# Kernel optimization log

Measured on AMD Instinct MI355X. Metric: run time of the kernel, lower is better.

## Reference

```python
import jax, jax.numpy as jnp
import numpy as np

D_MODEL = 256; HEADS = 8; DHEAD = D_MODEL // HEADS; FF = 2048
B, N = 2, 1024
T, H, W = 16, 128, 128
DS = (2, 8, 8)    # downsample_factor == offset_scale
KS = (4, 10, 10)  # offset kernel size


def layer_norm(x, w, b, eps=1e-5):
    mu = x.mean(-1, keepdims=True)
    var = ((x - mu) ** 2).mean(-1, keepdims=True)
    return (x - mu) * jax.lax.rsqrt(var + eps) * w + b


def mha_self(x, in_w, in_b, out_w, out_b):
    # torch nn.MultiheadAttention (batch_first), self-attention, eval mode
    Bq, Nq, C = x.shape
    qkv = x @ in_w.T + in_b
    q, k, v = jnp.split(qkv, 3, axis=-1)
    sh = lambda t: t.reshape(Bq, Nq, HEADS, DHEAD).transpose(0, 2, 1, 3)
    q, k, v = sh(q), sh(k), sh(v)
    att = jax.nn.softmax(jnp.einsum('bhnd,bhmd->bhnm', q, k) / np.sqrt(DHEAD).astype(np.float32), axis=-1)
    o = jnp.einsum('bhnm,bhmd->bhnd', att, v).transpose(0, 2, 1, 3).reshape(Bq, Nq, C)
    return o @ out_w.T + out_b


def grid_sample_3d(vol, coords):
    # vol: (G,C,T,H,W); coords: (G,L,3) in [-1,1], order (z,y,x)
    # trilinear, zeros padding, align_corners=False (matches F.grid_sample)
    G, C, Tv, Hv, Wv = vol.shape
    z = ((coords[..., 0] + 1.0) * Tv - 1.0) * 0.5
    y = ((coords[..., 1] + 1.0) * Hv - 1.0) * 0.5
    x = ((coords[..., 2] + 1.0) * Wv - 1.0) * 0.5
    z0f, y0f, x0f = jnp.floor(z), jnp.floor(y), jnp.floor(x)
    wz1, wy1, wx1 = z - z0f, y - y0f, x - x0f
    z0, y0, x0 = z0f.astype(jnp.int32), y0f.astype(jnp.int32), x0f.astype(jnp.int32)
    flat = vol.reshape(G, C, Tv * Hv * Wv)

    def gather(zi, yi, xi):
        valid = ((zi >= 0) & (zi < Tv) & (yi >= 0) & (yi < Hv) & (xi >= 0) & (xi < Wv))
        idx = (jnp.clip(zi, 0, Tv - 1) * Hv + jnp.clip(yi, 0, Hv - 1)) * Wv + jnp.clip(xi, 0, Wv - 1)
        vals = jnp.take_along_axis(flat, idx[:, None, :], axis=2)
        return vals * valid[:, None, :].astype(vol.dtype)

    out = jnp.zeros((G, C, coords.shape[1]), vol.dtype)
    for dz in (0, 1):
        for dy in (0, 1):
            for dx in (0, 1):
                w = ((wz1 if dz else 1 - wz1) * (wy1 if dy else 1 - wy1) * (wx1 if dx else 1 - wx1))
                out = out + gather(z0 + dz, y0 + dy, x0 + dx) * w[:, None, :]
    return out


def deform_attn(x, queries, q_w, off_w1, off_b1, off_w2, k_w, v_w, out_w, out_b):
    # DeformableAttention3D: offsets from grouped volume features via strided
    # depthwise conv, tanh*offset_scale, grid_sample of the full-res volume,
    # grouped k/v projections, per-head attention of N queries over L samples.
    Bx, C, Tv, Hv, Wv = x.shape
    g, d = HEADS, C // HEADS
    Nq = queries.shape[1]
    xg = x.reshape(Bx * g, d, Tv, Hv, Wv)
    pads = [((k - s) // 2, (k - s) // 2) for k, s in zip(KS, DS)]
    off = jax.lax.conv_general_dilated(xg, off_w1, window_strides=DS, padding=pads,
                                       dimension_numbers=('NCDHW', 'OIDHW', 'NCDHW'),
                                       feature_group_count=d)
    off = jax.nn.gelu(off + off_b1[None, :, None, None, None])
    off = jnp.einsum('oc,bcthw->bothw', off_w2, off)  # (BG,3,t,h,w)
    scale = jnp.asarray(DS, off.dtype)
    off = jnp.tanh(off) * scale[None, :, None, None, None]
    td, hd, wd = off.shape[2:]
    gz, gy, gx = jnp.meshgrid(jnp.arange(td), jnp.arange(hd), jnp.arange(wd), indexing='ij')
    base = jnp.stack([gz, gy, gx], 0).astype(off.dtype)
    norm = jnp.asarray([max(td - 1, 1), max(hd - 1, 1), max(wd - 1, 1)], off.dtype)
    vgrid = 2.0 * (base[None] + off) / norm[None, :, None, None, None] - 1.0
    coords = vgrid.transpose(0, 2, 3, 4, 1).reshape(Bx * g, -1, 3)  # (BG,L,3)
    kv = grid_sample_3d(xg, coords).reshape(Bx, g, d, -1)            # (B,g,d,L)
    k = jnp.einsum('gof,bgfl->bgol', k_w, kv)
    v = jnp.einsum('gof,bgfl->bgol', v_w, kv)
    q = (queries @ q_w.T).reshape(Bx, Nq, g, d).transpose(0, 2, 1, 3)
    attn = jax.nn.softmax(jnp.einsum('bgnd,bgdl->bgnl', q, k) / np.sqrt(d).astype(np.float32), axis=-1)
    o = jnp.einsum('bgnl,bgdl->bgnd', attn, v).transpose(0, 2, 1, 3).reshape(Bx, Nq, C)
    return o @ out_w.T + out_b, attn


def decoder_layer(query_tokens, global_tokens, p):
    # forward_post, use_pe='use_pe' with pos=None, dropout in eval mode
    t = query_tokens + mha_self(query_tokens, p['sa_in_w'], p['sa_in_b'], p['sa_out_w'], p['sa_out_b'])
    t = layer_norm(t, p['ln1_w'], p['ln1_b'])
    da, attn = deform_attn(global_tokens, t, p['q_w'], p['off_w1'], p['off_b1'], p['off_w2'],
                           p['k_w'], p['v_w'], p['da_out_w'], p['da_out_b'])
    t = layer_norm(t + da, p['ln2_w'], p['ln2_b'])
    ff = jax.nn.relu(t @ p['lin1_w'].T + p['lin1_b']) @ p['lin2_w'].T + p['lin2_b']
    t = layer_norm(t + ff, p['ln3_w'], p['ln3_b'])
    return t, attn


PARAM_NAMES = ['sa_in_w', 'sa_in_b', 'sa_out_w', 'sa_out_b', 'q_w', 'off_w1', 'off_b1', 'off_w2',
               'k_w', 'v_w', 'da_out_w', 'da_out_b', 'lin1_w', 'lin1_b', 'lin2_w', 'lin2_b',
               'ln1_w', 'ln1_b', 'ln2_w', 'ln2_b', 'ln3_w', 'ln3_b']


def setup_inputs() -> dict:
    key = jax.random.key(0)
    ks = jax.random.split(key, 16)
    s = 0.02
    f = jnp.float32
    return {
        'query_tokens': jax.random.normal(ks[0], (B, N, D_MODEL), f),
        'global_tokens': jax.random.normal(ks[1], (B, D_MODEL, T, H, W), f),
        'sa_in_w': jax.random.normal(ks[2], (3 * D_MODEL, D_MODEL), f) * s,
        'sa_in_b': jnp.zeros((3 * D_MODEL,), f),
        'sa_out_w': jax.random.normal(ks[3], (D_MODEL, D_MODEL), f) * s,
        'sa_out_b': jnp.zeros((D_MODEL,), f),
        'q_w': jax.random.normal(ks[4], (D_MODEL, D_MODEL), f) * s,
        'off_w1': jax.random.normal(ks[5], (DHEAD, 1) + KS, f) * s,
        'off_b1': jnp.zeros((DHEAD,), f),
        'off_w2': jax.random.normal(ks[6], (3, DHEAD), f) * s,
        'k_w': jax.random.normal(ks[7], (HEADS, DHEAD, DHEAD), f) * s,
        'v_w': jax.random.normal(ks[8], (HEADS, DHEAD, DHEAD), f) * s,
        'da_out_w': jax.random.normal(ks[9], (D_MODEL, D_MODEL), f) * s,
        'da_out_b': jnp.zeros((D_MODEL,), f),
        'lin1_w': jax.random.normal(ks[10], (FF, D_MODEL), f) * s,
        'lin1_b': jnp.zeros((FF,), f),
        'lin2_w': jax.random.normal(ks[11], (D_MODEL, FF), f) * s,
        'lin2_b': jnp.zeros((D_MODEL,), f),
        'ln1_w': jnp.ones((D_MODEL,), f), 'ln1_b': jnp.zeros((D_MODEL,), f),
        'ln2_w': jnp.ones((D_MODEL,), f), 'ln2_b': jnp.zeros((D_MODEL,), f),
        'ln3_w': jnp.ones((D_MODEL,), f), 'ln3_b': jnp.zeros((D_MODEL,), f),
    }


def reference(query_tokens, global_tokens, sa_in_w, sa_in_b, sa_out_w, sa_out_b, q_w, off_w1,
              off_b1, off_w2, k_w, v_w, da_out_w, da_out_b, lin1_w, lin1_b, lin2_w, lin2_b,
              ln1_w, ln1_b, ln2_w, ln2_b, ln3_w, ln3_b):
    p = dict(zip(PARAM_NAMES, (sa_in_w, sa_in_b, sa_out_w, sa_out_b, q_w, off_w1, off_b1, off_w2,
                               k_w, v_w, da_out_w, da_out_b, lin1_w, lin1_b, lin2_w, lin2_b,
                               ln1_w, ln1_b, ln2_w, ln2_b, ln3_w, ln3_b)))
    return decoder_layer(query_tokens, global_tokens, p)
```

## Files before the change

### kernel.cpp

```cpp
#include <hip/hip_runtime.h>
#include <hip/hip_bf16.h>

#define BQ 2
#define NQ 1024
#define CM 256
#define HEADS 8
#define DH 32
#define FFD 2048
#define TV 16
#define HV 128
#define WV 128
#define TD 8
#define HD 16
#define WD 16
#define LS 2048
#define NG 16
#define MROWS 2048

typedef __attribute__((ext_vector_type(8))) short bf16x8;
typedef __attribute__((ext_vector_type(4))) float f32x4;

__device__ __forceinline__ ushort f2bf(float x) {
  __hip_bfloat16 h = __float2bfloat16(x);
  return *(ushort*)&h;
}

template <bool RELU>
__global__ __launch_bounds__(256) void gemm_nt(const float* __restrict__ A,
                                               const float* __restrict__ Wt,
                                               const float* __restrict__ bias,
                                               const float* __restrict__ res,
                                               float* __restrict__ C,
                                               int M, int N, int K) {
  __shared__ float As[16 * 68];
  __shared__ float Ws[16 * 68];
  const int tm = threadIdx.x & 15;
  const int tn = threadIdx.x >> 4;
  const int m0 = blockIdx.x * 64, n0 = blockIdx.y * 64;
  const int lr = threadIdx.x >> 2;
  const int lk = (threadIdx.x & 3) * 4;
  float acc[4][4] = {};
  for (int k0 = 0; k0 < K; k0 += 16) {
    float4 a4 = *(const float4*)(A + (size_t)(m0 + lr) * K + k0 + lk);
    float4 w4 = *(const float4*)(Wt + (size_t)(n0 + lr) * K + k0 + lk);
    As[(lk + 0) * 68 + lr] = a4.x;
    As[(lk + 1) * 68 + lr] = a4.y;
    As[(lk + 2) * 68 + lr] = a4.z;
    As[(lk + 3) * 68 + lr] = a4.w;
    Ws[(lk + 0) * 68 + lr] = w4.x;
    Ws[(lk + 1) * 68 + lr] = w4.y;
    Ws[(lk + 2) * 68 + lr] = w4.z;
    Ws[(lk + 3) * 68 + lr] = w4.w;
    __syncthreads();
#pragma unroll
    for (int k = 0; k < 16; ++k) {
      float4 av = *(const float4*)&As[k * 68 + tm * 4];
      float4 wv = *(const float4*)&Ws[k * 68 + tn * 4];
      float a[4] = {av.x, av.y, av.z, av.w};
      float w[4] = {wv.x, wv.y, wv.z, wv.w};
#pragma unroll
      for (int i = 0; i < 4; ++i)
#pragma unroll
        for (int j = 0; j < 4; ++j) acc[i][j] += a[i] * w[j];
    }
    __syncthreads();
  }
#pragma unroll
  for (int i = 0; i < 4; ++i) {
    const int row = m0 + tm * 4 + i;
    const int col = n0 + tn * 4;
    float4 bv = bias ? *(const float4*)(bias + col) : make_float4(0.f, 0.f, 0.f, 0.f);
    float4 rv = res ? *(const float4*)(res + (size_t)row * N + col) : make_float4(0.f, 0.f, 0.f, 0.f);
    float4 o;
    o.x = acc[i][0] + bv.x + rv.x;
    o.y = acc[i][1] + bv.y + rv.y;
    o.z = acc[i][2] + bv.z + rv.z;
    o.w = acc[i][3] + bv.w + rv.w;
    if (RELU) {
      o.x = fmaxf(o.x, 0.f); o.y = fmaxf(o.y, 0.f);
      o.z = fmaxf(o.z, 0.f); o.w = fmaxf(o.w, 0.f);
    }
    *(float4*)(C + (size_t)row * N + col) = o;
  }
}

template <bool RELU>
__global__ __launch_bounds__(256) void gemm_nt128(const float* __restrict__ A,
                                                  const float* __restrict__ Wt,
                                                  const float* __restrict__ bias,
                                                  const float* __restrict__ res,
                                                  float* __restrict__ C,
                                                  int M, int N, int K) {
  __shared__ float As[8][132];
  __shared__ float Bs[8][132];
  const int tid = threadIdx.x;
  const int tm = tid & 15, tn = tid >> 4;
  const int m0 = blockIdx.x * 128, n0 = blockIdx.y * 128;
  const int lr = tid >> 1, lk = (tid & 1) * 4;
  float acc[8][8] = {};
  const float* Ap = A + (size_t)(m0 + lr) * K + lk;
  const float* Wp = Wt + (size_t)(n0 + lr) * K + lk;
  for (int k0 = 0; k0 < K; k0 += 8) {
    float4 a4 = *(const float4*)(Ap + k0);
    float4 w4 = *(const float4*)(Wp + k0);
    __syncthreads();
    As[lk + 0][lr] = a4.x; As[lk + 1][lr] = a4.y; As[lk + 2][lr] = a4.z; As[lk + 3][lr] = a4.w;
    Bs[lk + 0][lr] = w4.x; Bs[lk + 1][lr] = w4.y; Bs[lk + 2][lr] = w4.z; Bs[lk + 3][lr] = w4.w;
    __syncthreads();
#pragma unroll
    for (int k = 0; k < 8; ++k) {
      float4 a0 = *(const float4*)&As[k][tm * 8];
      float4 a1 = *(const float4*)&As[k][tm * 8 + 4];
      float4 w0 = *(const float4*)&Bs[k][tn * 8];
      float4 w1 = *(const float4*)&Bs[k][tn * 8 + 4];
      float av[8] = {a0.x, a0.y, a0.z, a0.w, a1.x, a1.y, a1.z, a1.w};
      float wv[8] = {w0.x, w0.y, w0.z, w0.w, w1.x, w1.y, w1.z, w1.w};
#pragma unroll
      for (int i = 0; i < 8; ++i)
#pragma unroll
        for (int j = 0; j < 8; ++j) acc[i][j] += av[i] * wv[j];
    }
  }
#pragma unroll
  for (int i = 0; i < 8; ++i) {
    const int row = m0 + tm * 8 + i;
#pragma unroll
    for (int jj = 0; jj < 2; ++jj) {
      const int col = n0 + tn * 8 + jj * 4;
      float4 o = make_float4(acc[i][jj * 4 + 0], acc[i][jj * 4 + 1],
                             acc[i][jj * 4 + 2], acc[i][jj * 4 + 3]);
      if (bias) {
        float4 bv = *(const float4*)(bias + col);
        o.x += bv.x; o.y += bv.y; o.z += bv.z; o.w += bv.w;
      }
      if (res) {
        float4 rv = *(const float4*)(res + (size_t)row * N + col);
        o.x += rv.x; o.y += rv.y; o.z += rv.z; o.w += rv.w;
      }
      if (RELU) {
        o.x = fmaxf(o.x, 0.f); o.y = fmaxf(o.y, 0.f);
        o.z = fmaxf(o.z, 0.f); o.w = fmaxf(o.w, 0.f);
      }
      *(float4*)(C + (size_t)row * N + col) = o;
    }
  }
}

__global__ __launch_bounds__(256) void castw_kernel(const float* __restrict__ w1,
                                                    const float* __restrict__ w2,
                                                    __hip_bfloat16* __restrict__ w1b,
                                                    __hip_bfloat16* __restrict__ w2b) {
  const int idx = blockIdx.x * 256 + threadIdx.x;
  const float4* src;
  __hip_bfloat16* dst;
  int off;
  if (idx < 131072) { src = (const float4*)w1; dst = w1b; off = idx; }
  else              { src = (const float4*)w2; dst = w2b; off = idx - 131072; }
  float4 v = src[off];
  dst[off * 4 + 0] = __float2bfloat16(v.x);
  dst[off * 4 + 1] = __float2bfloat16(v.y);
  dst[off * 4 + 2] = __float2bfloat16(v.z);
  dst[off * 4 + 3] = __float2bfloat16(v.w);
}

template <bool LIN1>
__global__ __launch_bounds__(256) void gemm_bf16_mfma(const ushort* __restrict__ A,
                                                      const ushort* __restrict__ B,
                                                      const float* __restrict__ bias,
                                                      __hip_bfloat16* __restrict__ Cbf,
                                                      float* __restrict__ Cf,
                                                      int M, int N, int K, int kslen) {
  __shared__ ushort Asm[128][40];
  __shared__ ushort Bsm[128][40];
  const int tid = threadIdx.x;
  const int lane = tid & 63, wave = tid >> 6;
  const int wr = wave >> 1, wc = wave & 1;
  const int m0 = blockIdx.x * 128, n0 = blockIdx.y * 128;
  const int kb = blockIdx.z * kslen;
  f32x4 acc[4][4] = {};

  const int r0 = tid >> 1, c0 = (tid & 1) * 16;
  for (int k0 = kb; k0 < kb + kslen; k0 += 32) {
    uint4 ar0 = *(const uint4*)(A + (size_t)(m0 + r0) * K + k0 + c0);
    uint4 ar1 = *(const uint4*)(A + (size_t)(m0 + r0) * K + k0 + c0 + 8);
    uint4 br0 = *(const uint4*)(B + (size_t)(n0 + r0) * K + k0 + c0);
    uint4 br1 = *(const uint4*)(B + (size_t)(n0 + r0) * K + k0 + c0 + 8);
    __syncthreads();
    *(uint4*)&Asm[r0][c0] = ar0;
    *(uint4*)&Asm[r0][c0 + 8] = ar1;
    *(uint4*)&Bsm[r0][c0] = br0;
    *(uint4*)&Bsm[r0][c0 + 8] = br1;
    __syncthreads();
    bf16x8 af[4], bfr[4];
#pragma unroll
    for (int mi = 0; mi < 4; ++mi)
      af[mi] = *(const bf16x8*)&Asm[wr * 64 + mi * 16 + (lane & 15)][(lane >> 4) * 8];
#pragma unroll
    for (int ni = 0; ni < 4; ++ni)
      bfr[ni] = *(const bf16x8*)&Bsm[wc * 64 + ni * 16 + (lane & 15)][(lane >> 4) * 8];
#pragma unroll
    for (int mi = 0; mi < 4; ++mi)
#pragma unroll
      for (int ni = 0; ni < 4; ++ni)
        acc[mi][ni] = __builtin_amdgcn_mfma_f32_16x16x32_bf16(af[mi], bfr[ni], acc[mi][ni], 0, 0, 0);
  }

  const int rbase = (lane >> 4) * 4;
  const int cl = lane & 15;
#pragma unroll
  for (int mi = 0; mi < 4; ++mi) {
    const int rowb = m0 + wr * 64 + mi * 16 + rbase;
#pragma unroll
    for (int ni = 0; ni < 4; ++ni) {
      const int col = n0 + wc * 64 + ni * 16 + cl;
      if (LIN1) {
        const float bv = bias[col];
#pragma unroll
        for (int reg = 0; reg < 4; ++reg) {
          float x = acc[mi][ni][reg] + bv;
          x = fmaxf(x, 0.f);
          Cbf[(size_t)(rowb + reg) * N + col] = __float2bfloat16(x);
        }
      } else {
        float* Pb = Cf + (size_t)blockIdx.z * M * N;
#pragma unroll
        for (int reg = 0; reg < 4; ++reg)
          Pb[(size_t)(rowb + reg) * N + col] = acc[mi][ni][reg];
      }
    }
  }
}

__global__ __launch_bounds__(256) void skred8_kernel(const float* __restrict__ P,
                                                     const float* __restrict__ bias,
                                                     const float* __restrict__ res,
                                                     float* __restrict__ C) {
  const int idx = blockIdx.x * 256 + threadIdx.x;
  const int col4 = idx & 63;
  const int row = idx >> 6;
  const float4* P4 = (const float4*)P;
  const int MN4 = MROWS * CM / 4;
  float4 s = make_float4(0.f, 0.f, 0.f, 0.f);
#pragma unroll
  for (int sl = 0; sl < 8; ++sl) {
    float4 p = P4[idx + sl * MN4];
    s.x += p.x; s.y += p.y; s.z += p.z; s.w += p.w;
  }
  float4 bv = ((const float4*)bias)[col4];
  float4 rv = ((const float4*)(res + (size_t)row * CM))[col4];
  s.x += bv.x + rv.x; s.y += bv.y + rv.y;
  s.z += bv.z + rv.z; s.w += bv.w + rv.w;
  ((float4*)C)[idx] = s;
}

#define SKC 64
#define SNC (NQ / SKC)
__global__ __launch_bounds__(256) void sa_flash_kernel(const float* __restrict__ qkv,
                                                       float* __restrict__ o) {
  __shared__ float Qs[16][36];
  __shared__ float Ks[SKC][36];
  __shared__ float Vs[SKC][36];
  __shared__ float Ps[16][68];
  __shared__ float Ored[8 * 16 * 32];

  const int swz = (blockIdx.x & 7) * 128 + (blockIdx.x >> 3);
  const int bh = swz >> 6, qt = swz & 63;
  const int n0 = qt * 16;
  const int b = bh >> 3, h = bh & 7;
  const int tid = threadIdx.x;
  const int lane = tid & 63, wave = tid >> 6;

  const float* rowbase = qkv + (size_t)b * NQ * 768 + h * DH;

  if (tid < 128) {
    const int r = tid >> 3, c4 = (tid & 7) * 4;
    *(float4*)&Qs[r][c4] = *(const float4*)(rowbase + (size_t)(n0 + r) * 768 + c4);
  }
  __syncthreads();

  const int dslot = (tid >> 3) & 7;
  const int kg = tid & 7;
  float ssum[4] = {0.f, 0.f, 0.f, 0.f};
  float o0[4] = {}, o1[4] = {}, o2[4] = {}, o3[4] = {};

#pragma unroll 1
  for (int c = 0; c < SNC; ++c) {
    {
      const int r0 = tid >> 3, c40 = (tid & 7) * 4;
      const int r1 = r0 + 32;
      *(float4*)&Ks[r0][c40] =
          *(const float4*)(rowbase + (size_t)(c * SKC + r0) * 768 + 256 + c40);
      *(float4*)&Ks[r1][c40] =
          *(const float4*)(rowbase + (size_t)(c * SKC + r1) * 768 + 256 + c40);
      *(float4*)&Vs[r0][c40] =
          *(const float4*)(rowbase + (size_t)(c * SKC + r0) * 768 + 512 + c40);
      *(float4*)&Vs[r1][c40] =
          *(const float4*)(rowbase + (size_t)(c * SKC + r1) * 768 + 512 + c40);
    }
    __syncthreads();
    float4 kr[8];
#pragma unroll
    for (int d4 = 0; d4 < 8; ++d4) kr[d4] = *(const float4*)&Ks[lane][d4 * 4];
#pragma unroll
    for (int qi = 0; qi < 4; ++qi) {
      const int q = wave * 4 + qi;
      float s = 0.f;
#pragma unroll
      for (int d4 = 0; d4 < 8; ++d4) {
        float4 q4 = *(const float4*)&Qs[q][d4 * 4];
        s += q4.x * kr[d4].x + q4.y * kr[d4].y + q4.z * kr[d4].z + q4.w * kr[d4].w;
      }
      const float e = __expf(s * 0.17677669529663687f);
      ssum[qi] += e;
      Ps[q][lane] = e;
    }
#pragma unroll
    for (int j = 0; j < 8; ++j) {
      const int kk = kg * 8 + j;
      float4 v4 = *(const float4*)&Vs[kk][dslot * 4];
      const float p0 = Ps[wave * 4 + 0][kk];
      const float p1 = Ps[wave * 4 + 1][kk];
      const float p2 = Ps[wave * 4 + 2][kk];
      const float p3 = Ps[wave * 4 + 3][kk];
      o0[0] += p0 * v4.x; o0[1] += p0 * v4.y; o0[2] += p0 * v4.z; o0[3] += p0 * v4.w;
      o1[0] += p1 * v4.x; o1[1] += p1 * v4.y; o1[2] += p1 * v4.z; o1[3] += p1 * v4.w;
      o2[0] += p2 * v4.x; o2[1] += p2 * v4.y; o2[2] += p2 * v4.z; o2[3] += p2 * v4.w;
      o3[0] += p3 * v4.x; o3[1] += p3 * v4.y; o3[2] += p3 * v4.z; o3[3] += p3 * v4.w;
    }
    __syncthreads();
  }

  float inv[4];
#pragma unroll
  for (int qi = 0; qi < 4; ++qi) {
    float ss = ssum[qi];
#pragma unroll
    for (int off = 32; off > 0; off >>= 1) ss += __shfl_xor(ss, off, 64);
    inv[qi] = 1.f / ss;
  }

#pragma unroll
  for (int j = 0; j < 4; ++j) {
    Ored[kg * (16 * 32) + (wave * 4 + 0) * 32 + dslot * 4 + j] = o0[j] * inv[0];
    Ored[kg * (16 * 32) + (wave * 4 + 1) * 32 + dslot * 4 + j] = o1[j] * inv[1];
    Ored[kg * (16 * 32) + (wave * 4 + 2) * 32 + dslot * 4 + j] = o2[j] * inv[2];
    Ored[kg * (16 * 32) + (wave * 4 + 3) * 32 + dslot * 4 + j] = o3[j] * inv[3];
  }
  __syncthreads();
#pragma unroll
  for (int i = 0; i < 2; ++i) {
    const int idx = tid * 2 + i;
    const int q = idx >> 5, d = idx & 31;
    float s = 0.f;
#pragma unroll
    for (int k = 0; k < 8; ++k) s += Ored[k * (16 * 32) + q * 32 + d];
    o[((size_t)(b * NQ + n0 + q)) * CM + h * DH + d] = s;
  }
}

__global__ __launch_bounds__(256) void ln_kernel(const float* __restrict__ in,
                                                 const float* __restrict__ w,
                                                 const float* __restrict__ b,
                                                 float* __restrict__ out,
                                                 __hip_bfloat16* __restrict__ out_bf) {
  const int wv = threadIdx.x >> 6, lane = threadIdx.x & 63;
  const int row = blockIdx.x * 4 + wv;
  float4 v = ((const float4*)(in + (size_t)row * CM))[lane];
  float s = v.x + v.y + v.z + v.w;
#pragma unroll
  for (int off = 32; off > 0; off >>= 1) s += __shfl_xor(s, off, 64);
  const float mu = s * (1.f / 256.f);
  float dx = v.x - mu, dy = v.y - mu, dz = v.z - mu, dw = v.w - mu;
  float q = dx * dx + dy * dy + dz * dz + dw * dw;
#pragma unroll
  for (int off = 32; off > 0; off >>= 1) q += __shfl_xor(q, off, 64);
  const float r = rsqrtf(q * (1.f / 256.f) + 1e-5f);
  float4 wv4 = ((const float4*)w)[lane];
  float4 bv4 = ((const float4*)b)[lane];
  float4 o;
  o.x = dx * r * wv4.x + bv4.x;
  o.y = dy * r * wv4.y + bv4.y;
  o.z = dz * r * wv4.z + bv4.z;
  o.w = dw * r * wv4.w + bv4.w;
  ((float4*)(out + (size_t)row * CM))[lane] = o;
  if (out_bf) {
    __hip_bfloat16* op = out_bf + (size_t)row * CM + lane * 4;
    op[0] = __float2bfloat16(o.x);
    op[1] = __float2bfloat16(o.y);
    op[2] = __float2bfloat16(o.z);
    op[3] = __float2bfloat16(o.w);
  }
}

__global__ __launch_bounds__(256) void conv_off6_kernel(const float* __restrict__ gt,
                                                        const float* __restrict__ w1,
                                                        const float* __restrict__ b1,
                                                        float* __restrict__ off1) {
  const int bid = blockIdx.x;
  const int yh = bid & 1, zh = (bid >> 1) & 1, cid = bid >> 2;
  const int c = cid & 31;
  const int tid = threadIdx.x;
  const int xo = tid & 15;
  const int yo8 = (tid >> 4) & 7;
  const int zoq = tid >> 7;
  __shared__ float wsm[400];
  __shared__ float pl[2][66 * 128];
  for (int i = tid; i < 400; i += 256) wsm[i] = w1[c * 400 + i];

  const float* __restrict__ xp = gt + (size_t)cid * (TV * HV * WV);
  const int zo0 = zh * 4 + zoq * 2;
  const int ygbase = yh * 64 - 1;
  const int zlo = zh ? 7 : 0;
  const int zhi = zh ? 15 : 8;
  float acc0 = 0.f, acc1 = 0.f;
  float4 rv[9];

  {
    const float* __restrict__ zp = xp + (size_t)zlo * (HV * WV);
#pragma unroll
    for (int k = 0; k < 9; ++k) {
      const int i = tid + k * 256;
      if (i < 2112) {
        const int r = i >> 5, f = i & 31;
        const int y = ygbase + r;
        float4 v = make_float4(0.f, 0.f, 0.f, 0.f);
        if ((unsigned)y < 128u) v = *(const float4*)(zp + y * WV + 4 * f);
        const int fp = f ^ ((r >> 3) & 3);
        *(float4*)&pl[0][r * 128 + 4 * fp] = v;
      }
    }
  }
  __syncthreads();

  int cur = 0;
#pragma unroll 1
  for (int z = zlo; z <= zhi; ++z) {
    if (z < zhi) {
      const float* __restrict__ zp = xp + (size_t)(z + 1) * (HV * WV);
#pragma unroll
      for (int k = 0; k < 9; ++k) {
        const int i = tid + k * 256;
        rv[k] = make_float4(0.f, 0.f, 0.f, 0.f);
        if (i < 2112) {
          const int y = ygbase + (i >> 5);
          if ((unsigned)y < 128u) rv[k] = *(const float4*)(zp + y * WV + 4 * (i & 31));
        }
      }
    }
    {
      const int kzA = z + 1 - 2 * zo0;
      const int kzB = kzA - 2;
      const bool actA = (unsigned)kzA <= 3u;
      const bool actB = (unsigned)kzB <= 3u;
      if (actA || actB) {
        const float* __restrict__ wrA = wsm + (actA ? kzA : 0) * 100;
        const float* __restrict__ wrB = wsm + (actB ? kzB : 0) * 100;
#pragma unroll 2
        for (int ky = 0; ky < 10; ++ky) {
          const int r = yo8 * 8 + ky;
          const int s = (r >> 3) & 3;
          const float* __restrict__ rp = &pl[cur][r * 128];
          const float4 a0 = *(const float4*)&rp[((2 * xo) ^ s) * 4];
          const float4 a1 = *(const float4*)&rp[((2 * xo + 1) ^ s) * 4];
          float left = 0.f, right = 0.f;
          if (xo > 0) {
            const int cc = 8 * xo - 1;
            left = rp[((((cc >> 2) ^ s)) << 2) | (cc & 3)];
          }
          if (xo < 15) {
            const int cc = 8 * xo + 8;
            right = rp[((((cc >> 2) ^ s)) << 2) | (cc & 3)];
          }
          if (actA) {
            const float* __restrict__ w = wrA + ky * 10;
            acc0 += w[0] * left + w[1] * a0.x + w[2] * a0.y + w[3] * a0.z + w[4] * a0.w +
                    w[5] * a1.x + w[6] * a1.y + w[7] * a1.z + w[8] * a1.w + w[9] * right;
          }
          if (actB) {
            const float* __restrict__ w = wrB + ky * 10;
            acc1 += w[0] * left + w[1] * a0.x + w[2] * a0.y + w[3] * a0.z + w[4] * a0.w +
                    w[5] * a1.x + w[6] * a1.y + w[7] * a1.z + w[8] * a1.w + w[9] * right;
          }
        }
      }
    }
    if (z < zhi) {
#pragma unroll
      for (int k = 0; k < 9; ++k) {
        const int i = tid + k * 256;
        if (i < 2112) {
          const int r = i >> 5, f = i & 31;
          const int fp = f ^ ((r >> 3) & 3);
          *(float4*)&pl[cur ^ 1][r * 128 + 4 * fp] = rv[k];
        }
      }
    }
    __syncthreads();
    cur ^= 1;
  }

  const float bias = b1[c];
  const int yout = yh * 8 + yo8;
  {
    float a = acc0 + bias;
    const float u = 0.7978845608028654f * (a + 0.044715f * a * a * a);
    const float gv = 0.5f * a * (1.f + tanhf(u));
    off1[((size_t)cid * TD + zo0) * (HD * WD) + yout * WD + xo] = gv;
  }
  {
    float a = acc1 + bias;
    const float u = 0.7978845608028654f * (a + 0.044715f * a * a * a);
    const float gv = 0.5f * a * (1.f + tanhf(u));
    off1[((size_t)cid * TD + zo0 + 1) * (HD * WD) + yout * WD + xo] = gv;
  }
}

__global__ __launch_bounds__(256) void offproj_kernel(const float* __restrict__ off1,
                                                      const float* __restrict__ w2,
                                                      float* __restrict__ pc) {
  const int gid = blockIdx.x * 256 + threadIdx.x;
  const int bg = gid >> 11, sp = gid & 2047;
  const float* base = off1 + (size_t)bg * 32 * LS + sp;
  float o0 = 0.f, o1 = 0.f, o2 = 0.f;
#pragma unroll
  for (int c = 0; c < 32; ++c) {
    const float v = base[(size_t)c * LS];
    o0 += w2[c] * v;
    o1 += w2[32 + c] * v;
    o2 += w2[64 + c] * v;
  }
  const int gz = sp >> 8, gy = (sp >> 4) & 15, gx = sp & 15;
  const float oz = tanhf(o0) * 2.f;
  const float oy = tanhf(o1) * 8.f;
  const float ox = tanhf(o2) * 8.f;
  float* p = pc + (size_t)gid * 3;
  p[0] = ((float)gz + oz) * (16.f / 7.f) - 0.5f;
  p[1] = ((float)gy + oy) * (128.f / 15.f) - 0.5f;
  p[2] = ((float)gx + ox) * (128.f / 15.f) - 0.5f;
}

__global__ __launch_bounds__(256) void gsample_kernel(const float* __restrict__ gt,
                                                      const float* __restrict__ pc,
                                                      const float* __restrict__ kw,
                                                      const float* __restrict__ vw,
                                                      float* __restrict__ kbuf,
                                                      float* __restrict__ vbuf) {
  __shared__ float kvv[8][33];
  __shared__ float kws[32][33], vws[32][33];
  const int swz = (blockIdx.x & 7) * 512 + (blockIdx.x >> 3);
  const int bg = swz >> 8, l0 = (swz & 255) * 8;
  const int g = bg & 7;
  const int s = threadIdx.x >> 5, c = threadIdx.x & 31;
  for (int i = threadIdx.x; i < 1024; i += 256) {
    kws[i >> 5][i & 31] = kw[g * 1024 + i];
    vws[i >> 5][i & 31] = vw[g * 1024 + i];
  }
  const int l = l0 + s;
  const float* p = pc + ((size_t)bg * LS + l) * 3;
  const float pz = p[0], py = p[1], px = p[2];
  const float zf = floorf(pz), yf = floorf(py), xf = floorf(px);
  const int z0 = (int)zf, y0 = (int)yf, x0 = (int)xf;
  const float fz = pz - zf, fy = py - yf, fx = px - xf;
  const float* vp = gt + (size_t)(bg * 32 + c) * (TV * HV * WV);
  float acc = 0.f;
#pragma unroll
  for (int dz = 0; dz < 2; ++dz) {
    const int z = z0 + dz;
    if ((unsigned)z >= (unsigned)TV) continue;
    const float wz = dz ? fz : 1.f - fz;
#pragma unroll
    for (int dy = 0; dy < 2; ++dy) {
      const int y = y0 + dy;
      if ((unsigned)y >= (unsigned)HV) continue;
      const float wzy = wz * (dy ? fy : 1.f - fy);
#pragma unroll
      for (int dx = 0; dx < 2; ++dx) {
        const int x = x0 + dx;
        if ((unsigned)x >= (unsigned)WV) continue;
        acc += wzy * (dx ? fx : 1.f - fx) * vp[((size_t)z * HV + y) * WV + x];
      }
    }
  }
  kvv[s][c] = acc;
  __syncthreads();
  float ka = 0.f, va = 0.f;
#pragma unroll
  for (int f = 0; f < 32; ++f) {
    const float kv = kvv[s][f];
    ka += kws[c][f] * kv;
    va += vws[c][f] * kv;
  }
  kbuf[((size_t)bg * LS + l) * 32 + c] = ka;
  vbuf[((size_t)bg * LS + l) * 32 + c] = va;
}

__global__ __launch_bounds__(256) void dattn_mfma_kernel(const float* __restrict__ qb,
                                                         const float* __restrict__ kbuf,
                                                         const float* __restrict__ vbuf,
                                                         float* __restrict__ da_o,
                                                         float* __restrict__ attn_out) {
  __shared__ ushort Qs[32][40];
  __shared__ ushort Ks[64][40];
  __shared__ ushort Vst[32][72];
  __shared__ ushort Ps[32][72];
  __shared__ float ssum_lds[4][16];
  __shared__ float invs[32];

  const int swz = (blockIdx.x & 7) * 64 + (blockIdx.x >> 3);
  const int bg = swz >> 5, qt = swz & 31;
  const int n0 = qt * 32;
  const int b = bg >> 3, g = bg & 7;
  const int tid = threadIdx.x;
  const int lane = tid & 63, wave = tid >> 6;
  const int qh = wave >> 1, kh = wave & 1;

  const float* kB = kbuf + (size_t)bg * LS * 32;
  const float* vB = vbuf + (size_t)bg * LS * 32;

  {
    const int r = tid >> 3, c4 = (tid & 7) * 4;
    float4 q4 = *(const float4*)(qb + ((size_t)(b * NQ + n0 + r)) * CM + g * DH + c4);
    Qs[r][c4 + 0] = f2bf(q4.x); Qs[r][c4 + 1] = f2bf(q4.y);
    Qs[r][c4 + 2] = f2bf(q4.z); Qs[r][c4 + 3] = f2bf(q4.w);
  }

  float ssum[4] = {0.f, 0.f, 0.f, 0.f};
  f32x4 accp = {};

  const int krow = tid >> 2, kc4 = (tid & 3) * 8;
  const int arow = lane & 15;
  const int ak8 = (lane >> 4) * 8;
  const int rrow = (lane >> 4) * 4;
  const int ccol = lane & 15;

#pragma unroll 1
  for (int c = 0; c < 32; ++c) {
    __syncthreads();
    {
      float4 k0 = *(const float4*)(kB + (size_t)(c * 64 + krow) * 32 + kc4);
      float4 k1 = *(const float4*)(kB + (size_t)(c * 64 + krow) * 32 + kc4 + 4);
      float4 v0 = *(const float4*)(vB + (size_t)(c * 64 + krow) * 32 + kc4);
      float4 v1 = *(const float4*)(vB + (size_t)(c * 64 + krow) * 32 + kc4 + 4);
      Ks[krow][kc4 + 0] = f2bf(k0.x); Ks[krow][kc4 + 1] = f2bf(k0.y);
      Ks[krow][kc4 + 2] = f2bf(k0.z); Ks[krow][kc4 + 3] = f2bf(k0.w);
      Ks[krow][kc4 + 4] = f2bf(k1.x); Ks[krow][kc4 + 5] = f2bf(k1.y);
      Ks[krow][kc4 + 6] = f2bf(k1.z); Ks[krow][kc4 + 7] = f2bf(k1.w);
      Vst[kc4 + 0][krow] = f2bf(v0.x); Vst[kc4 + 1][krow] = f2bf(v0.y);
      Vst[kc4 + 2][krow] = f2bf(v0.z); Vst[kc4 + 3][krow] = f2bf(v0.w);
      Vst[kc4 + 4][krow] = f2bf(v1.x); Vst[kc4 + 5][krow] = f2bf(v1.y);
      Vst[kc4 + 6][krow] = f2bf(v1.z); Vst[kc4 + 7][krow] = f2bf(v1.w);
    }
    __syncthreads();
    bf16x8 aq = *(const bf16x8*)&Qs[qh * 16 + arow][ak8];
#pragma unroll
    for (int ti = 0; ti < 2; ++ti) {
      const int t = kh * 2 + ti;
      bf16x8 bk = *(const bf16x8*)&Ks[t * 16 + arow][ak8];
      f32x4 sc = {};
      sc = __builtin_amdgcn_mfma_f32_16x16x32_bf16(aq, bk, sc, 0, 0, 0);
#pragma unroll
      for (int reg = 0; reg < 4; ++reg) {
        const float e = __expf(sc[reg] * 0.17677669529663687f);
        ssum[reg] += e;
        attn_out[((size_t)(bg * NQ + n0 + qh * 16 + rrow + reg)) * LS + c * 64 + t * 16 + ccol] = e;
        Ps[qh * 16 + rrow + reg][t * 16 + ccol] = f2bf(e);
      }
    }
    __syncthreads();
    {
      bf16x8 ap0 = *(const bf16x8*)&Ps[qh * 16 + arow][ak8];
      bf16x8 bv0 = *(const bf16x8*)&Vst[kh * 16 + arow][ak8];
      accp = __builtin_amdgcn_mfma_f32_16x16x32_bf16(ap0, bv0, accp, 0, 0, 0);
      bf16x8 ap1 = *(const bf16x8*)&Ps[qh * 16 + arow][32 + ak8];
      bf16x8 bv1 = *(const bf16x8*)&Vst[kh * 16 + arow][32 + ak8];
      accp = __builtin_amdgcn_mfma_f32_16x16x32_bf16(ap1, bv1, accp, 0, 0, 0);
    }
  }

#pragma unroll
  for (int reg = 0; reg < 4; ++reg) {
    float s = ssum[reg];
#pragma unroll
    for (int off = 1; off < 16; off <<= 1) s += __shfl_xor(s, off, 64);
    if ((lane & 15) == 0) ssum_lds[wave][rrow + reg] = s;
  }
  __syncthreads();
  if (tid < 32) {
    const int qh2 = tid >> 4, r = tid & 15;
    invs[tid] = 1.f / (ssum_lds[qh2 * 2][r] + ssum_lds[qh2 * 2 + 1][r]);
  }
  __syncthreads();

#pragma unroll
  for (int reg = 0; reg < 4; ++reg) {
    const int q = qh * 16 + rrow + reg;
    da_o[((size_t)(b * NQ + n0 + q)) * CM + g * DH + kh * 16 + ccol] = accp[reg] * invs[q];
  }

  const int nrow = tid >> 3;
  const float qinv = invs[nrow];
  float4* arow4 = (float4*)(attn_out + ((size_t)(bg * NQ + n0 + nrow)) * LS);
#pragma unroll 8
  for (int j = 0; j < 64; ++j) {
    const int col = (tid & 7) + j * 8;
    float4 a = arow4[col];
    a.x *= qinv; a.y *= qinv; a.z *= qinv; a.w *= qinv;
    arow4[col] = a;
  }
}

extern "C" void kernel_launch(void* const* d_in, const int* in_sizes, int n_in,
                              void* d_out, int out_size, void* d_ws, size_t ws_size,
                              hipStream_t stream) {
  const float* query    = (const float*)d_in[0];
  const float* gt       = (const float*)d_in[1];
  const float* sa_in_w  = (const float*)d_in[2];
  const float* sa_in_b  = (const float*)d_in[3];
  const float* sa_out_w = (const float*)d_in[4];
  const float* sa_out_b = (const float*)d_in[5];
  const float* q_w      = (const float*)d_in[6];
  const float* off_w1   = (const float*)d_in[7];
  const float* off_b1   = (const float*)d_in[8];
  const float* off_w2   = (const float*)d_in[9];
  const float* k_w      = (const float*)d_in[10];
  const float* v_w      = (const float*)d_in[11];
  const float* da_out_w = (const float*)d_in[12];
  const float* da_out_b = (const float*)d_in[13];
  const float* lin1_w   = (const float*)d_in[14];
  const float* lin1_b   = (const float*)d_in[15];
  const float* lin2_w   = (const float*)d_in[16];
  const float* lin2_b   = (const float*)d_in[17];
  const float* ln1_w    = (const float*)d_in[18];
  const float* ln1_b    = (const float*)d_in[19];
  const float* ln2_w    = (const float*)d_in[20];
  const float* ln2_b    = (const float*)d_in[21];
  const float* ln3_w    = (const float*)d_in[22];
  const float* ln3_b    = (const float*)d_in[23];

  float* ws = (float*)d_ws;
  float* t1      = ws + 0;
  float* t2      = ws + 524288;
  float* off1    = ws + 1048576;
  float* pcoords = ws + 2097152;
  float* k_buf   = ws + 2195456;
  float* v_buf   = ws + 3244032;
  float* q_buf   = ws + 4292608;
  float* da_o    = ws + 4816896;
  float* qkv_buf = ws + 5341184;
  float* sa_o    = ws + 6914048;
  float* t0      = ws + 7438336;
  float* u2      = ws + 7962624;
  float* skp     = ws + 8486912;
  float* u3      = ws + 6291456;
  __hip_bfloat16* t2bf   = (__hip_bfloat16*)(ws + 12681216);
  __hip_bfloat16* w1bf   = (__hip_bfloat16*)(ws + 12943360);
  __hip_bfloat16* w2bf   = (__hip_bfloat16*)(ws + 13205504);
  __hip_bfloat16* hbufbf = (__hip_bfloat16*)(ws + 13467648);

  float* out_t    = (float*)d_out;
  float* out_attn = out_t + (size_t)MROWS * CM;

  castw_kernel<<<1024, 256, 0, stream>>>(lin1_w, lin2_w, w1bf, w2bf);
  gemm_nt128<false><<<dim3(MROWS / 128, 768 / 128), 256, 0, stream>>>(
      query, sa_in_w, sa_in_b, nullptr, qkv_buf, MROWS, 768, CM);
  sa_flash_kernel<<<1024, 256, 0, stream>>>(qkv_buf, sa_o);
  gemm_nt<false><<<dim3(MROWS / 64, CM / 64), 256, 0, stream>>>(
      sa_o, sa_out_w, sa_out_b, query, t0, MROWS, CM, CM);
  ln_kernel<<<512, 256, 0, stream>>>(t0, ln1_w, ln1_b, t1, nullptr);
  conv_off6_kernel<<<2048, 256, 0, stream>>>(gt, off_w1, off_b1, off1);
  offproj_kernel<<<128, 256, 0, stream>>>(off1, off_w2, pcoords);
  gsample_kernel<<<4096, 256, 0, stream>>>(gt, pcoords, k_w, v_w, k_buf, v_buf);
  gemm_nt<false><<<dim3(MROWS / 64, CM / 64), 256, 0, stream>>>(
      t1, q_w, nullptr, nullptr, q_buf, MROWS, CM, CM);
  dattn_mfma_kernel<<<512, 256, 0, stream>>>(q_buf, k_buf, v_buf, da_o, out_attn);
  gemm_nt<false><<<dim3(MROWS / 64, CM / 64), 256, 0, stream>>>(
      da_o, da_out_w, da_out_b, t1, u2, MROWS, CM, CM);
  ln_kernel<<<512, 256, 0, stream>>>(u2, ln2_w, ln2_b, t2, t2bf);
  gemm_bf16_mfma<true><<<dim3(MROWS / 128, FFD / 128, 1), 256, 0, stream>>>(
      (const ushort*)t2bf, (const ushort*)w1bf, lin1_b, hbufbf, nullptr,
      MROWS, FFD, CM, CM);
  gemm_bf16_mfma<false><<<dim3(MROWS / 128, CM / 128, 8), 256, 0, stream>>>(
      (const ushort*)hbufbf, (const ushort*)w2bf, nullptr, nullptr, skp,
      MROWS, CM, FFD, FFD / 8);
  skred8_kernel<<<512, 256, 0, stream>>>(skp, lin2_b, t2, u3);
  ln_kernel<<<512, 256, 0, stream>>>(u3, ln3_w, ln3_b, out_t, nullptr);
}
```

Measured before the change: 541.3 us.

## Move self-attention QKV projection and attention core to bf16 MFMA

Replaces the fp32 SIMT QKV projection GEMM with the existing bf16 MFMA GEMM, adding a bias-only epilogue and extending the cast kernel so it also converts the query tokens and in-projection weights to bf16. Rewrites the self-attention kernel to compute QK^T and PV with 16x16x32 bf16 MFMA instructions, using 32-query tiles and 512 blocks. The aim is to remove the scalar FMA cost of the attention and projection. In exchange it loses precision by rounding Q, K, V and the probabilities to bf16, and it still skips max subtraction in the softmax.

New measurement: 448.4 us. 17.2% less time.

```diff
diff --git a/kernel.cpp b/kernel.cpp
--- a/kernel.cpp
+++ b/kernel.cpp
@@ -84,78 +84,22 @@
   }
 }
 
-template <bool RELU>
-__global__ __launch_bounds__(256) void gemm_nt128(const float* __restrict__ A,
-                                                  const float* __restrict__ Wt,
-                                                  const float* __restrict__ bias,
-                                                  const float* __restrict__ res,
-                                                  float* __restrict__ C,
-                                                  int M, int N, int K) {
-  __shared__ float As[8][132];
-  __shared__ float Bs[8][132];
-  const int tid = threadIdx.x;
-  const int tm = tid & 15, tn = tid >> 4;
-  const int m0 = blockIdx.x * 128, n0 = blockIdx.y * 128;
-  const int lr = tid >> 1, lk = (tid & 1) * 4;
-  float acc[8][8] = {};
-  const float* Ap = A + (size_t)(m0 + lr) * K + lk;
-  const float* Wp = Wt + (size_t)(n0 + lr) * K + lk;
-  for (int k0 = 0; k0 < K; k0 += 8) {
-    float4 a4 = *(const float4*)(Ap + k0);
-    float4 w4 = *(const float4*)(Wp + k0);
-    __syncthreads();
-    As[lk + 0][lr] = a4.x; As[lk + 1][lr] = a4.y; As[lk + 2][lr] = a4.z; As[lk + 3][lr] = a4.w;
-    Bs[lk + 0][lr] = w4.x; Bs[lk + 1][lr] = w4.y; Bs[lk + 2][lr] = w4.z; Bs[lk + 3][lr] = w4.w;
-    __syncthreads();
-#pragma unroll
-    for (int k = 0; k < 8; ++k) {
-      float4 a0 = *(const float4*)&As[k][tm * 8];
-      float4 a1 = *(const float4*)&As[k][tm * 8 + 4];
-      float4 w0 = *(const float4*)&Bs[k][tn * 8];
-      float4 w1 = *(const float4*)&Bs[k][tn * 8 + 4];
-      float av[8] = {a0.x, a0.y, a0.z, a0.w, a1.x, a1.y, a1.z, a1.w};
-      float wv[8] = {w0.x, w0.y, w0.z, w0.w, w1.x, w1.y, w1.z, w1.w};
-#pragma unroll
-      for (int i = 0; i < 8; ++i)
-#pragma unroll
-        for (int j = 0; j < 8; ++j) acc[i][j] += av[i] * wv[j];
-    }
-  }
-#pragma unroll
-  for (int i = 0; i < 8; ++i) {
-    const int row = m0 + tm * 8 + i;
-#pragma unroll
-    for (int jj = 0; jj < 2; ++jj) {
-      const int col = n0 + tn * 8 + jj * 4;
-      float4 o = make_float4(acc[i][jj * 4 + 0], acc[i][jj * 4 + 1],
-                             acc[i][jj * 4 + 2], acc[i][jj * 4 + 3]);
-      if (bias) {
-        float4 bv = *(const float4*)(bias + col);
-        o.x += bv.x; o.y += bv.y; o.z += bv.z; o.w += bv.w;
-      }
-      if (res) {
-        float4 rv = *(const float4*)(res + (size_t)row * N + col);
-        o.x += rv.x; o.y += rv.y; o.z += rv.z; o.w += rv.w;
-      }
-      if (RELU) {
-        o.x = fmaxf(o.x, 0.f); o.y = fmaxf(o.y, 0.f);
-        o.z = fmaxf(o.z, 0.f); o.w = fmaxf(o.w, 0.f);
-      }
-      *(float4*)(C + (size_t)row * N + col) = o;
-    }
-  }
-}
-
-__global__ __launch_bounds__(256) void castw_kernel(const float* __restrict__ w1,
-                                                    const float* __restrict__ w2,
-                                                    __hip_bfloat16* __restrict__ w1b,
-                                                    __hip_bfloat16* __restrict__ w2b) {
+__global__ __launch_bounds__(256) void castw4_kernel(const float* __restrict__ q,
+                                                     const float* __restrict__ sw,
+                                                     const float* __restrict__ w1,
+                                                     const float* __restrict__ w2,
+                                                     __hip_bfloat16* __restrict__ qb,
+                                                     __hip_bfloat16* __restrict__ swb,
+                                                     __hip_bfloat16* __restrict__ w1b,
+                                                     __hip_bfloat16* __restrict__ w2b) {
   const int idx = blockIdx.x * 256 + threadIdx.x;
   const float4* src;
   __hip_bfloat16* dst;
   int off;
-  if (idx < 131072) { src = (const float4*)w1; dst = w1b; off = idx; }
-  else              { src = (const float4*)w2; dst = w2b; off = idx - 131072; }
+  if (idx < 131072)      { src = (const float4*)q;  dst = qb;  off = idx; }
+  else if (idx < 180224) { src = (const float4*)sw; dst = swb; off = idx - 131072; }
+  else if (idx < 311296) { src = (const float4*)w1; dst = w1b; off = idx - 180224; }
+  else                   { src = (const float4*)w2; dst = w2b; off = idx - 311296; }
   float4 v = src[off];
   dst[off * 4 + 0] = __float2bfloat16(v.x);
   dst[off * 4 + 1] = __float2bfloat16(v.y);
@@ -163,7 +107,7 @@
   dst[off * 4 + 3] = __float2bfloat16(v.w);
 }
 
-template <bool LIN1>
+template <int EPI>
 __global__ __launch_bounds__(256) void gemm_bf16_mfma(const ushort* __restrict__ A,
                                                       const ushort* __restrict__ B,
                                                       const float* __restrict__ bias,
@@ -213,7 +157,7 @@
 #pragma unroll
     for (int ni = 0; ni < 4; ++ni) {
       const int col = n0 + wc * 64 + ni * 16 + cl;
-      if (LIN1) {
+      if (EPI == 0) {
         const float bv = bias[col];
 #pragma unroll
         for (int reg = 0; reg < 4; ++reg) {
@@ -221,11 +165,16 @@
           x = fmaxf(x, 0.f);
           Cbf[(size_t)(rowb + reg) * N + col] = __float2bfloat16(x);
         }
-      } else {
+      } else if (EPI == 1) {
         float* Pb = Cf + (size_t)blockIdx.z * M * N;
 #pragma unroll
         for (int reg = 0; reg < 4; ++reg)
           Pb[(size_t)(rowb + reg) * N + col] = acc[mi][ni][reg];
+      } else {
+        const float bv = bias[col];
+#pragma unroll
+        for (int reg = 0; reg < 4; ++reg)
+          Cf[(size_t)(rowb + reg) * N + col] = acc[mi][ni][reg] + bv;
       }
     }
   }
@@ -253,108 +202,104 @@
   ((float4*)C)[idx] = s;
 }
 
-#define SKC 64
-#define SNC (NQ / SKC)
-__global__ __launch_bounds__(256) void sa_flash_kernel(const float* __restrict__ qkv,
-                                                       float* __restrict__ o) {
-  __shared__ float Qs[16][36];
-  __shared__ float Ks[SKC][36];
-  __shared__ float Vs[SKC][36];
-  __shared__ float Ps[16][68];
-  __shared__ float Ored[8 * 16 * 32];
-
-  const int swz = (blockIdx.x & 7) * 128 + (blockIdx.x >> 3);
-  const int bh = swz >> 6, qt = swz & 63;
-  const int n0 = qt * 16;
+__global__ __launch_bounds__(256) void sa_mfma_kernel(const float* __restrict__ qkv,
+                                                      float* __restrict__ o) {
+  __shared__ ushort Qs[32][40];
+  __shared__ ushort Ks[64][40];
+  __shared__ ushort Vst[32][72];
+  __shared__ ushort Ps[32][72];
+  __shared__ float ssum_lds[4][16];
+  __shared__ float invs[32];
+
+  const int swz = (blockIdx.x & 7) * 64 + (blockIdx.x >> 3);
+  const int bh = swz >> 5, qt = swz & 31;
+  const int n0 = qt * 32;
   const int b = bh >> 3, h = bh & 7;
   const int tid = threadIdx.x;
   const int lane = tid & 63, wave = tid >> 6;
+  const int qh = wave >> 1, kh = wave & 1;
 
   const float* rowbase = qkv + (size_t)b * NQ * 768 + h * DH;
 
-  if (tid < 128) {
+  {
     const int r = tid >> 3, c4 = (tid & 7) * 4;
-    *(float4*)&Qs[r][c4] = *(const float4*)(rowbase + (size_t)(n0 + r) * 768 + c4);
+    float4 q4 = *(const float4*)(rowbase + (size_t)(n0 + r) * 768 + c4);
+    Qs[r][c4 + 0] = f2bf(q4.x); Qs[r][c4 + 1] = f2bf(q4.y);
+    Qs[r][c4 + 2] = f2bf(q4.z); Qs[r][c4 + 3] = f2bf(q4.w);
+  }
+
+  float ssum[4] = {0.f, 0.f, 0.f, 0.f};
+  f32x4 accp = {};
+
+  const int krow = tid >> 2, kc4 = (tid & 3) * 8;
+  const int arow = lane & 15;
+  const int ak8 = (lane >> 4) * 8;
+  const int rrow = (lane >> 4) * 4;
+  const int ccol = lane & 15;
+
+#pragma unroll 1
+  for (int c = 0; c < 16; ++c) {
+    __syncthreads();
+    {
+      const float* kp = rowbase + (size_t)(c * 64 + krow) * 768 + 256 + kc4;
+      const float* vp = rowbase + (size_t)(c * 64 + krow) * 768 + 512 + kc4;
+      float4 k0 = *(const float4*)kp;
+      float4 k1 = *(const float4*)(kp + 4);
+      float4 v0 = *(const float4*)vp;
+      float4 v1 = *(const float4*)(vp + 4);
+      Ks[krow][kc4 + 0] = f2bf(k0.x); Ks[krow][kc4 + 1] = f2bf(k0.y);
+      Ks[krow][kc4 + 2] = f2bf(k0.z); Ks[krow][kc4 + 3] = f2bf(k0.w);
+      Ks[krow][kc4 + 4] = f2bf(k1.x); Ks[krow][kc4 + 5] = f2bf(k1.y);
+      Ks[krow][kc4 + 6] = f2bf(k1.z); Ks[krow][kc4 + 7] = f2bf(k1.w);
+      Vst[kc4 + 0][krow] = f2bf(v0.x); Vst[kc4 + 1][krow] = f2bf(v0.y);
+      Vst[kc4 + 2][krow] = f2bf(v0.z); Vst[kc4 + 3][krow] = f2bf(v0.w);
+      Vst[kc4 + 4][krow] = f2bf(v1.x); Vst[kc4 + 5][krow] = f2bf(v1.y);
+      Vst[kc4 + 6][krow] = f2bf(v1.z); Vst[kc4 + 7][krow] = f2bf(v1.w);
+    }
+    __syncthreads();
+    bf16x8 aq = *(const bf16x8*)&Qs[qh * 16 + arow][ak8];
+#pragma unroll
+    for (int ti = 0; ti < 2; ++ti) {
+      const int t = kh * 2 + ti;
+      bf16x8 bk = *(const bf16x8*)&Ks[t * 16 + arow][ak8];
+      f32x4 sc = {};
+      sc = __builtin_amdgcn_mfma_f32_16x16x32_bf16(aq, bk, sc, 0, 0, 0);
+#pragma unroll
+      for (int reg = 0; reg < 4; ++reg) {
+        const float e = __expf(sc[reg] * 0.17677669529663687f);
+        ssum[reg] += e;
+        Ps[qh * 16 + rrow + reg][t * 16 + ccol] = f2bf(e);
+      }
+    }
+    __syncthreads();
+    {
+      bf16x8 ap0 = *(const bf16x8*)&Ps[qh * 16 + arow][ak8];
+      bf16x8 bv0 = *(const bf16x8*)&Vst[kh * 16 + arow][ak8];
+      accp = __builtin_amdgcn_mfma_f32_16x16x32_bf16(ap0, bv0, accp, 0, 0, 0);
+      bf16x8 ap1 = *(const bf16x8*)&Ps[qh * 16 + arow][32 + ak8];
+      bf16x8 bv1 = *(const bf16x8*)&Vst[kh * 16 + arow][32 + ak8];
+      accp = __builtin_amdgcn_mfma_f32_16x16x32_bf16(ap1, bv1, accp, 0, 0, 0);
+    }
+  }
+
+#pragma unroll
+  for (int reg = 0; reg < 4; ++reg) {
+    float s = ssum[reg];
+#pragma unroll
+    for (int off = 1; off < 16; off <<= 1) s += __shfl_xor(s, off, 64);
+    if ((lane & 15) == 0) ssum_lds[wave][rrow + reg] = s;
   }
   __syncthreads();
-
-  const int dslot = (tid >> 3) & 7;
-  const int kg = tid & 7;
-  float ssum[4] = {0.f, 0.f, 0.f, 0.f};
-  float o0[4] = {}, o1[4] = {}, o2[4] = {}, o3[4] = {};
-
-#pragma unroll 1
-  for (int c = 0; c < SNC; ++c) {
-    {
-      const int r0 = tid >> 3, c40 = (tid & 7) * 4;
-      const int r1 = r0 + 32;
-      *(float4*)&Ks[r0][c40] =
-          *(const float4*)(rowbase + (size_t)(c * SKC + r0) * 768 + 256 + c40);
-      *(float4*)&Ks[r1][c40] =
-          *(const float4*)(rowbase + (size_t)(c * SKC + r1) * 768 + 256 + c40);
-      *(float4*)&Vs[r0][c40] =
-          *(const float4*)(rowbase + (size_t)(c * SKC + r0) * 768 + 512 + c40);
-      *(float4*)&Vs[r1][c40] =
-          *(const float4*)(rowbase + (size_t)(c * SKC + r1) * 768 + 512 + c40);
-    }
-    __syncthreads();
-    float4 kr[8];
-#pragma unroll
-    for (int d4 = 0; d4 < 8; ++d4) kr[d4] = *(const float4*)&Ks[lane][d4 * 4];
-#pragma unroll
-    for (int qi = 0; qi < 4; ++qi) {
-      const int q = wave * 4 + qi;
-      float s = 0.f;
-#pragma unroll
-      for (int d4 = 0; d4 < 8; ++d4) {
-        float4 q4 = *(const float4*)&Qs[q][d4 * 4];
-        s += q4.x * kr[d4].x + q4.y * kr[d4].y + q4.z * kr[d4].z + q4.w * kr[d4].w;
-      }
-      const float e = __expf(s * 0.17677669529663687f);
-      ssum[qi] += e;
-      Ps[q][lane] = e;
-    }
-#pragma unroll
-    for (int j = 0; j < 8; ++j) {
-      const int kk = kg * 8 + j;
-      float4 v4 = *(const float4*)&Vs[kk][dslot * 4];
-      const float p0 = Ps[wave * 4 + 0][kk];
-      const float p1 = Ps[wave * 4 + 1][kk];
-      const float p2 = Ps[wave * 4 + 2][kk];
-      const float p3 = Ps[wave * 4 + 3][kk];
-      o0[0] += p0 * v4.x; o0[1] += p0 * v4.y; o0[2] += p0 * v4.z; o0[3] += p0 * v4.w;
-      o1[0] += p1 * v4.x; o1[1] += p1 * v4.y; o1[2] += p1 * v4.z; o1[3] += p1 * v4.w;
-      o2[0] += p2 * v4.x; o2[1] += p2 * v4.y; o2[2] += p2 * v4.z; o2[3] += p2 * v4.w;
-      o3[0] += p3 * v4.x; o3[1] += p3 * v4.y; o3[2] += p3 * v4.z; o3[3] += p3 * v4.w;
-    }
-    __syncthreads();
-  }
-
-  float inv[4];
-#pragma unroll
-  for (int qi = 0; qi < 4; ++qi) {
-    float ss = ssum[qi];
-#pragma unroll
-    for (int off = 32; off > 0; off >>= 1) ss += __shfl_xor(ss, off, 64);
-    inv[qi] = 1.f / ss;
-  }
-
-#pragma unroll
-  for (int j = 0; j < 4; ++j) {
-    Ored[kg * (16 * 32) + (wave * 4 + 0) * 32 + dslot * 4 + j] = o0[j] * inv[0];
-    Ored[kg * (16 * 32) + (wave * 4 + 1) * 32 + dslot * 4 + j] = o1[j] * inv[1];
-    Ored[kg * (16 * 32) + (wave * 4 + 2) * 32 + dslot * 4 + j] = o2[j] * inv[2];
-    Ored[kg * (16 * 32) + (wave * 4 + 3) * 32 + dslot * 4 + j] = o3[j] * inv[3];
+  if (tid < 32) {
+    const int qh2 = tid >> 4, r = tid & 15;
+    invs[tid] = 1.f / (ssum_lds[qh2 * 2][r] + ssum_lds[qh2 * 2 + 1][r]);
   }
   __syncthreads();
-#pragma unroll
-  for (int i = 0; i < 2; ++i) {
-    const int idx = tid * 2 + i;
-    const int q = idx >> 5, d = idx & 31;
-    float s = 0.f;
-#pragma unroll
-    for (int k = 0; k < 8; ++k) s += Ored[k * (16 * 32) + q * 32 + d];
-    o[((size_t)(b * NQ + n0 + q)) * CM + h * DH + d] = s;
+
+#pragma unroll
+  for (int reg = 0; reg < 4; ++reg) {
+    const int q = qh * 16 + rrow + reg;
+    o[((size_t)(b * NQ + n0 + q)) * CM + h * DH + kh * 16 + ccol] = accp[reg] * invs[q];
   }
 }
 
@@ -752,6 +697,8 @@
   float* u2      = ws + 7962624;
   float* skp     = ws + 8486912;
   float* u3      = ws + 6291456;
+  __hip_bfloat16* qbf    = (__hip_bfloat16*)(ws + 8486912);
+  __hip_bfloat16* sawbf  = (__hip_bfloat16*)(ws + 8749056);
   __hip_bfloat16* t2bf   = (__hip_bfloat16*)(ws + 12681216);
   __hip_bfloat16* w1bf   = (__hip_bfloat16*)(ws + 12943360);
   __hip_bfloat16* w2bf   = (__hip_bfloat16*)(ws + 13205504);
@@ -760,10 +707,12 @@
   float* out_t    = (float*)d_out;
   float* out_attn = out_t + (size_t)MROWS * CM;
 
-  castw_kernel<<<1024, 256, 0, stream>>>(lin1_w, lin2_w, w1bf, w2bf);
-  gemm_nt128<false><<<dim3(MROWS / 128, 768 / 128), 256, 0, stream>>>(
-      query, sa_in_w, sa_in_b, nullptr, qkv_buf, MROWS, 768, CM);
-  sa_flash_kernel<<<1024, 256, 0, stream>>>(qkv_buf, sa_o);
+  castw4_kernel<<<1728, 256, 0, stream>>>(query, sa_in_w, lin1_w, lin2_w,
+                                          qbf, sawbf, w1bf, w2bf);
+  gemm_bf16_mfma<2><<<dim3(MROWS / 128, 768 / 128, 1), 256, 0, stream>>>(
+      (const ushort*)qbf, (const ushort*)sawbf, sa_in_b, nullptr, qkv_buf,
+      MROWS, 768, CM, CM);
+  sa_mfma_kernel<<<512, 256, 0, stream>>>(qkv_buf, sa_o);
   gemm_nt<false><<<dim3(MROWS / 64, CM / 64), 256, 0, stream>>>(
       sa_o, sa_out_w, sa_out_b, query, t0, MROWS, CM, CM);
   ln_kernel<<<512, 256, 0, stream>>>(t0, ln1_w, ln1_b, t1, nullptr);
@@ -776,10 +725,10 @@
   gemm_nt<false><<<dim3(MROWS / 64, CM / 64), 256, 0, stream>>>(
       da_o, da_out_w, da_out_b, t1, u2, MROWS, CM, CM);
   ln_kernel<<<512, 256, 0, stream>>>(u2, ln2_w, ln2_b, t2, t2bf);
-  gemm_bf16_mfma<true><<<dim3(MROWS / 128, FFD / 128, 1), 256, 0, stream>>>(
+  gemm_bf16_mfma<0><<<dim3(MROWS / 128, FFD / 128, 1), 256, 0, stream>>>(
       (const ushort*)t2bf, (const ushort*)w1bf, lin1_b, hbufbf, nullptr,
       MROWS, FFD, CM, CM);
-  gemm_bf16_mfma<false><<<dim3(MROWS / 128, CM / 128, 8), 256, 0, stream>>>(
+  gemm_bf16_mfma<1><<<dim3(MROWS / 128, CM / 128, 8), 256, 0, stream>>>(
       (const ushort*)hbufbf, (const ushort*)w2bf, nullptr, nullptr, skp,
       MROWS, CM, FFD, FFD / 8);
   skred8_kernel<<<512, 256, 0, stream>>>(skp, lin2_b, t2, u3);
```
